# Kernel tuning notes

Measured on AMD Instinct MI355X. Metric: run time of the kernel, lower is better.

Reference implementation:

```python
import jax, jax.numpy as jnp
import numpy as np

UNITS = 512
CONN = 512          # input feature dim (connections)
DEND_SIZE = 16
SEQL = CONN // DEND_SIZE  # 32 dendrite segments per unit
BATCH = 512


def _make_dendrites(units, conn, dsize, seed=0):
    # Per-unit random permutation of input indices, grouped into contiguous
    # dendrites of size dsize -> segment id in [0, seql) for every input index.
    rng = np.random.default_rng(seed)
    seql = conn // dsize
    seg = np.empty((units, conn), dtype=np.int32)
    for u in range(units):
        perm = rng.permutation(conn)
        for s in range(seql):
            seg[u, perm[dsize * s:dsize * (s + 1)]] = s
    return seg


def setup_inputs() -> dict:
    key = jax.random.key(0)
    k1, k2, k3, k4 = jax.random.split(key, 4)
    x = jax.random.normal(k1, (BATCH, CONN), dtype=jnp.float32)
    # weight_twice & not uniqueW -> per-unit scalar input weight, shape [1, units]
    kernel = jax.random.uniform(k2, (1, UNITS), dtype=jnp.float32, minval=5e-5, maxval=0.1)
    # per-(segment, unit) dendritic weight, shape [seql, units]
    dendriticW = jax.random.uniform(k3, (SEQL, UNITS), dtype=jnp.float32, minval=5e-5, maxval=0.1)
    bias = jax.random.normal(k4, (UNITS,), dtype=jnp.float32) * 0.05
    dendrites = jnp.asarray(_make_dendrites(UNITS, CONN, DEND_SIZE))  # [units, conn] int32
    return {"x": x, "kernel": kernel, "dendriticW": dendriticW,
            "bias": bias, "dendrites": dendrites}


def reference(x, kernel, dendriticW, bias, dendrites):
    # x: [batch, conn]; dendrites: [units, conn] segment ids in [0, SEQL)
    xT = x.T  # [conn, batch]
    # per-unit gather + unsorted_segment_sum over connections -> [units, seql, batch]
    segsum = jax.vmap(lambda seg: jax.ops.segment_sum(xT, seg, num_segments=SEQL))(dendrites)
    # weight_twice: per-unit scalar input weight (kernel broadcast over conn)
    segsum = segsum * kernel[0][:, None, None]
    # dendritic weighting + reduction over segments -> [batch, units]
    out = jnp.einsum('usb,su->bu', segsum, dendriticW) + bias
    return jax.nn.relu(out)
```

## Files before the change

kernel.cpp:

```cpp
#include <hip/hip_runtime.h>
#include <hip/hip_bf16.h>

#define UNITS 512
#define CONN  512
#define SEQL  32

typedef __hip_bfloat16 bf16;
typedef __attribute__((ext_vector_type(8))) short short8;
typedef __attribute__((ext_vector_type(4))) float floatx4;


union cv8 { bf16 h[8]; short8 v; };

__global__ __launch_bounds__(256) void prep(
    const float* __restrict__ kern,
    const float* __restrict__ dW,
    const int*   __restrict__ dend,
    const float* __restrict__ x,
    bf16* __restrict__ W,
    bf16* __restrict__ xb,
    int nxthreads)
{
    __shared__ float table[4][SEQL];
    const int tid = blockIdx.x * 256 + threadIdx.x;
    const int WTHREADS = UNITS * (CONN / 8);

    if (tid < WTHREADS) {
        const int u    = tid >> 6;
        const int lane = threadIdx.x & 63;
        const int wid  = threadIdx.x >> 6;
        if (lane < SEQL)
            table[wid][lane] = dW[lane * UNITS + u];
        __syncthreads();

        const int c0 = lane * 8;
        const float kv = kern[u];
        const int4 s0 = ((const int4*)(dend + u * CONN + c0))[0];
        const int4 s1 = ((const int4*)(dend + u * CONN + c0))[1];
        const int segs[8] = {s0.x, s0.y, s0.z, s0.w, s1.x, s1.y, s1.z, s1.w};
        cv8 w;
#pragma unroll
        for (int i = 0; i < 8; ++i)
            w.h[i] = __float2bfloat16(kv * table[wid][segs[i]]);
        *(short8*)(W + u * CONN + c0) = w.v;
    } else {
        __syncthreads();
        const int t = tid - WTHREADS;
        if (t < nxthreads) {
            const float4 f0 = ((const float4*)x)[t * 2];
            const float4 f1 = ((const float4*)x)[t * 2 + 1];
            cv8 a;
            a.h[0] = __float2bfloat16(f0.x); a.h[1] = __float2bfloat16(f0.y);
            a.h[2] = __float2bfloat16(f0.z); a.h[3] = __float2bfloat16(f0.w);
            a.h[4] = __float2bfloat16(f1.x); a.h[5] = __float2bfloat16(f1.y);
            a.h[6] = __float2bfloat16(f1.z); a.h[7] = __float2bfloat16(f1.w);
            *(short8*)(xb + t * 8) = a.v;
        }
    }
}

__global__ __launch_bounds__(64) void gemm_mfma(
    const bf16*  __restrict__ xb,
    const bf16*  __restrict__ W,
    const float* __restrict__ bias,
    float* __restrict__ out)
{
    const int lane = threadIdx.x;
    const int ut = blockIdx.x * 16;
    const int bt = blockIdx.y * 16;
    const int m = lane & 15;
    const int q = lane >> 4;

    const bf16* xrow = xb + (size_t)(bt + m) * CONN + q * 8;
    const bf16* wrow = W  + (size_t)(ut + m) * CONN + q * 8;

    floatx4 acc = {0.f, 0.f, 0.f, 0.f};
#pragma unroll
    for (int k = 0; k < CONN; k += 32) {
        const short8 a = *(const short8*)(xrow + k);
        const short8 b = *(const short8*)(wrow + k);
        acc = __builtin_amdgcn_mfma_f32_16x16x32_bf16(a, b, acc, 0, 0, 0);
    }

    const float bu = bias[ut + m];
#pragma unroll
    for (int r = 0; r < 4; ++r) {
        float v = acc[r] + bu;
        v = v > 0.f ? v : 0.f;
        out[(size_t)(bt + q * 4 + r) * UNITS + ut + m] = v;
    }
}

__device__ __forceinline__ short8 cvt8(const float* p) {
    const float4 f0 = ((const float4*)p)[0];
    const float4 f1 = ((const float4*)p)[1];
    cv8 a;
    a.h[0] = __float2bfloat16(f0.x); a.h[1] = __float2bfloat16(f0.y);
    a.h[2] = __float2bfloat16(f0.z); a.h[3] = __float2bfloat16(f0.w);
    a.h[4] = __float2bfloat16(f1.x); a.h[5] = __float2bfloat16(f1.y);
    a.h[6] = __float2bfloat16(f1.z); a.h[7] = __float2bfloat16(f1.w);
    return a.v;
}

__global__ __launch_bounds__(256) void dendriter_fused_mfma(
    const float* __restrict__ x, const float* __restrict__ kern,
    const float* __restrict__ dW, const float* __restrict__ bias,
    const int* __restrict__ dend, float* __restrict__ out)
{
    __shared__ short8 wl[16][65];
    const int t  = threadIdx.x;
    const int ut = blockIdx.x * 16;
    const int bt = blockIdx.y * 64;
    {
        const int ul  = t >> 4;
        const int cg0 = (t & 15) * 4;
        const int u   = ut + ul;
        const float kv = kern[u];
        const int4* dp = (const int4*)(dend + u * CONN + cg0 * 8);
#pragma unroll
        for (int j = 0; j < 4; ++j) {
            const int4 s0 = dp[2 * j];
            const int4 s1 = dp[2 * j + 1];
            const int segs[8] = {s0.x, s0.y, s0.z, s0.w, s1.x, s1.y, s1.z, s1.w};
            cv8 w;
#pragma unroll
            for (int i = 0; i < 8; ++i)
                w.h[i] = __float2bfloat16(kv * dW[segs[i] * UNITS + u]);
            const int cg = cg0 + j;
            wl[cg >> 2][ul | ((cg & 3) << 4)] = w.v;
        }
    }
    __syncthreads();

    const int lane = t & 63;
    const int wv   = t >> 6;
    const int m = lane & 15;
    const int q = lane >> 4;
    const int btw = bt + wv * 16;
    const float* xrow = x + (size_t)(btw + m) * CONN + q * 8;
    floatx4 acc = {0.f, 0.f, 0.f, 0.f};
#pragma unroll
    for (int kb = 0; kb < 16; ++kb) {
        const short8 a = cvt8(xrow + kb * 32);
        const short8 b = wl[kb][lane];
        acc = __builtin_amdgcn_mfma_f32_16x16x32_bf16(a, b, acc, 0, 0, 0);
    }
    const float bu = bias[ut + m];
#pragma unroll
    for (int r = 0; r < 4; ++r) {
        float v = acc[r] + bu;
        v = v > 0.f ? v : 0.f;
        out[(size_t)(btw + q * 4 + r) * UNITS + ut + m] = v;
    }
}

extern "C" void kernel_launch(void* const* d_in, const int* in_sizes, int n_in,
                              void* d_out, int out_size, void* d_ws, size_t ws_size,
                              hipStream_t stream) {
    const float* x    = (const float*)d_in[0];
    const float* kern = (const float*)d_in[1];
    const float* dW   = (const float*)d_in[2];
    const float* bias = (const float*)d_in[3];
    const int*   dend = (const int*)  d_in[4];
    float* out = (float*)d_out;

    const int batch = in_sizes[0] / CONN;
    const size_t w_bytes  = (size_t)UNITS * CONN * sizeof(bf16);
    const size_t xb_bytes = (size_t)batch * CONN * sizeof(bf16);
    const int nxthreads = batch * CONN / 8;

    if (ws_size >= w_bytes + xb_bytes) {
        bf16* W  = (bf16*)d_ws;
        bf16* xb = W + (size_t)UNITS * CONN;
        prep<<<(UNITS * CONN / 8 + nxthreads + 255) / 256, 256, 0, stream>>>(
            kern, dW, dend, x, W, xb, nxthreads);
        gemm_mfma<<<dim3(UNITS / 16, batch / 16), 64, 0, stream>>>(xb, W, bias, out);
    } else {
        dendriter_fused_mfma<<<dim3(UNITS / 16, batch / 64), 256, 0, stream>>>(
            x, kern, dW, bias, dend, out);
    }
}
```

Measured before the change: 66.31 us.

## Replace prep+GEMM two-kernel path with single fused kernel using LDS weight table

Drops the workspace path, which ran a prep kernel to build bf16 W and x and then a separate small-tile GEMM. A single fused kernel now builds the per-unit weight tile in LDS and runs MFMA directly on fp32 x converted in registers. The fused kernel also prefetches all of x's A-fragments before the weight-build phase, and precomputes kern*dW into a shared table instead of doing scattered global gathers. This removes one launch and the round trip of intermediates through global memory, but every block recomputes its weight tile and register pressure rises from holding 16 fragments.

After: 67.13 us. Within noise of the previous version (+1.2%).

```diff
diff --git a/kernel.cpp b/kernel.cpp
--- a/kernel.cpp
+++ b/kernel.cpp
@@ -12,85 +12,6 @@
 
 union cv8 { bf16 h[8]; short8 v; };
 
-__global__ __launch_bounds__(256) void prep(
-    const float* __restrict__ kern,
-    const float* __restrict__ dW,
-    const int*   __restrict__ dend,
-    const float* __restrict__ x,
-    bf16* __restrict__ W,
-    bf16* __restrict__ xb,
-    int nxthreads)
-{
-    __shared__ float table[4][SEQL];
-    const int tid = blockIdx.x * 256 + threadIdx.x;
-    const int WTHREADS = UNITS * (CONN / 8);
-
-    if (tid < WTHREADS) {
-        const int u    = tid >> 6;
-        const int lane = threadIdx.x & 63;
-        const int wid  = threadIdx.x >> 6;
-        if (lane < SEQL)
-            table[wid][lane] = dW[lane * UNITS + u];
-        __syncthreads();
-
-        const int c0 = lane * 8;
-        const float kv = kern[u];
-        const int4 s0 = ((const int4*)(dend + u * CONN + c0))[0];
-        const int4 s1 = ((const int4*)(dend + u * CONN + c0))[1];
-        const int segs[8] = {s0.x, s0.y, s0.z, s0.w, s1.x, s1.y, s1.z, s1.w};
-        cv8 w;
-#pragma unroll
-        for (int i = 0; i < 8; ++i)
-            w.h[i] = __float2bfloat16(kv * table[wid][segs[i]]);
-        *(short8*)(W + u * CONN + c0) = w.v;
-    } else {
-        __syncthreads();
-        const int t = tid - WTHREADS;
-        if (t < nxthreads) {
-            const float4 f0 = ((const float4*)x)[t * 2];
-            const float4 f1 = ((const float4*)x)[t * 2 + 1];
-            cv8 a;
-            a.h[0] = __float2bfloat16(f0.x); a.h[1] = __float2bfloat16(f0.y);
-            a.h[2] = __float2bfloat16(f0.z); a.h[3] = __float2bfloat16(f0.w);
-            a.h[4] = __float2bfloat16(f1.x); a.h[5] = __float2bfloat16(f1.y);
-            a.h[6] = __float2bfloat16(f1.z); a.h[7] = __float2bfloat16(f1.w);
-            *(short8*)(xb + t * 8) = a.v;
-        }
-    }
-}
-
-__global__ __launch_bounds__(64) void gemm_mfma(
-    const bf16*  __restrict__ xb,
-    const bf16*  __restrict__ W,
-    const float* __restrict__ bias,
-    float* __restrict__ out)
-{
-    const int lane = threadIdx.x;
-    const int ut = blockIdx.x * 16;
-    const int bt = blockIdx.y * 16;
-    const int m = lane & 15;
-    const int q = lane >> 4;
-
-    const bf16* xrow = xb + (size_t)(bt + m) * CONN + q * 8;
-    const bf16* wrow = W  + (size_t)(ut + m) * CONN + q * 8;
-
-    floatx4 acc = {0.f, 0.f, 0.f, 0.f};
-#pragma unroll
-    for (int k = 0; k < CONN; k += 32) {
-        const short8 a = *(const short8*)(xrow + k);
-        const short8 b = *(const short8*)(wrow + k);
-        acc = __builtin_amdgcn_mfma_f32_16x16x32_bf16(a, b, acc, 0, 0, 0);
-    }
-
-    const float bu = bias[ut + m];
-#pragma unroll
-    for (int r = 0; r < 4; ++r) {
-        float v = acc[r] + bu;
-        v = v > 0.f ? v : 0.f;
-        out[(size_t)(bt + q * 4 + r) * UNITS + ut + m] = v;
-    }
-}
-
 __device__ __forceinline__ short8 cvt8(const float* p) {
     const float4 f0 = ((const float4*)p)[0];
     const float4 f1 = ((const float4*)p)[1];
@@ -102,21 +23,43 @@
     return a.v;
 }
 
-__global__ __launch_bounds__(256) void dendriter_fused_mfma(
-    const float* __restrict__ x, const float* __restrict__ kern,
-    const float* __restrict__ dW, const float* __restrict__ bias,
-    const int* __restrict__ dend, float* __restrict__ out)
+__global__ __launch_bounds__(256) void dendriter_fused_v2(
+    const float* __restrict__ x,
+    const float* __restrict__ kern,
+    const float* __restrict__ dW,
+    const float* __restrict__ bias,
+    const int*   __restrict__ dend,
+    float* __restrict__ out)
 {
+    __shared__ float  table[16][SEQL];
     __shared__ short8 wl[16][65];
+
     const int t  = threadIdx.x;
     const int ut = blockIdx.x * 16;
     const int bt = blockIdx.y * 64;
+
+    const int lane = t & 63;
+    const int wv   = t >> 6;
+    const int m    = lane & 15;
+    const int q    = lane >> 4;
+    const int btw  = bt + wv * 16;
+    const float* xrow = x + (size_t)(btw + m) * CONN + q * 8;
+    short8 afr[16];
+#pragma unroll
+    for (int kb = 0; kb < 16; ++kb)
+        afr[kb] = cvt8(xrow + kb * 32);
+
+#pragma unroll
+    for (int e = t; e < 16 * SEQL; e += 256) {
+        const int seg = e >> 4, ul = e & 15;
+        table[ul][seg] = kern[ut + ul] * dW[seg * UNITS + ut + ul];
+    }
+    __syncthreads();
+
     {
         const int ul  = t >> 4;
         const int cg0 = (t & 15) * 4;
-        const int u   = ut + ul;
-        const float kv = kern[u];
-        const int4* dp = (const int4*)(dend + u * CONN + cg0 * 8);
+        const int4* dp = (const int4*)(dend + (size_t)(ut + ul) * CONN + cg0 * 8);
 #pragma unroll
         for (int j = 0; j < 4; ++j) {
             const int4 s0 = dp[2 * j];
@@ -125,26 +68,19 @@
             cv8 w;
 #pragma unroll
             for (int i = 0; i < 8; ++i)
-                w.h[i] = __float2bfloat16(kv * dW[segs[i] * UNITS + u]);
+                w.h[i] = __float2bfloat16(table[ul][segs[i]]);
             const int cg = cg0 + j;
             wl[cg >> 2][ul | ((cg & 3) << 4)] = w.v;
         }
     }
     __syncthreads();
 
-    const int lane = t & 63;
-    const int wv   = t >> 6;
-    const int m = lane & 15;
-    const int q = lane >> 4;
-    const int btw = bt + wv * 16;
-    const float* xrow = x + (size_t)(btw + m) * CONN + q * 8;
     floatx4 acc = {0.f, 0.f, 0.f, 0.f};
 #pragma unroll
-    for (int kb = 0; kb < 16; ++kb) {
-        const short8 a = cvt8(xrow + kb * 32);
-        const short8 b = wl[kb][lane];
-        acc = __builtin_amdgcn_mfma_f32_16x16x32_bf16(a, b, acc, 0, 0, 0);
-    }
+    for (int kb = 0; kb < 16; ++kb)
+        acc = __builtin_amdgcn_mfma_f32_16x16x32_bf16(afr[kb], wl[kb][lane],
+                                                      acc, 0, 0, 0);
+
     const float bu = bias[ut + m];
 #pragma unroll
     for (int r = 0; r < 4; ++r) {
@@ -165,18 +101,8 @@
     float* out = (float*)d_out;
 
     const int batch = in_sizes[0] / CONN;
-    const size_t w_bytes  = (size_t)UNITS * CONN * sizeof(bf16);
-    const size_t xb_bytes = (size_t)batch * CONN * sizeof(bf16);
-    const int nxthreads = batch * CONN / 8;
+    (void)d_ws; (void)ws_size;
 
-    if (ws_size >= w_bytes + xb_bytes) {
-        bf16* W  = (bf16*)d_ws;
-        bf16* xb = W + (size_t)UNITS * CONN;
-        prep<<<(UNITS * CONN / 8 + nxthreads + 255) / 256, 256, 0, stream>>>(
-            kern, dW, dend, x, W, xb, nxthreads);
-        gemm_mfma<<<dim3(UNITS / 16, batch / 16), 64, 0, stream>>>(xb, W, bias, out);
-    } else {
-        dendriter_fused_mfma<<<dim3(UNITS / 16, batch / 64), 256, 0, stream>>>(
-            x, kern, dW, bias, dend, out);
-    }
+    dendriter_fused_v2<<<dim3(UNITS / 16, batch / 64), 256, 0, stream>>>(
+        x, kern, dW, bias, dend, out);
 }
```
